# Kernel optimization log

Hardware: AMD Instinct MI355X
Metric: run time of the kernel (lower is better)

## Reference

```python
import jax, jax.numpy as jnp
import numpy as np

EPS = 1e-9          # nr.projection eps
EXPANSION = 0.5     # expansion_parts
Z_THRESH = 5.0      # interaction_threshold
B, NS, NO, P, KS, KO = 256, 10475, 65536, 8, 1024, 2048


def _make_cam_Ks(rng):
    # replicate __init__: focal = focal / bboxes[:,2:] * [192,256]; K /= 256
    wh = rng.uniform(100.0, 300.0, size=(B, 2)).astype(np.float32)
    f = 5000.0 / wh * np.array([192.0, 256.0], dtype=np.float32)
    K = np.tile(np.eye(3, dtype=np.float32), (B, 1, 1))
    K[:, 0, 0] = f[:, 0]
    K[:, 1, 1] = f[:, 1]
    K[:, 0, 2] = K[:, 1, 2] = 128.0
    return jnp.asarray(K / 256.0)


def setup_inputs() -> dict:
    key = jax.random.key(0)
    k1, k2, k3, k4 = jax.random.split(key, 4)
    rng = np.random.default_rng(0)
    return {
        "smpl_v": jax.random.normal(k1, (B, NS, 3), dtype=jnp.float32),
        "object_v": jax.random.normal(k2, (B, NO, 3), dtype=jnp.float32),
        "cam_Ks": _make_cam_Ks(rng),
        "smpl_part_idx": jax.random.randint(k3, (P, KS), 0, NS, dtype=jnp.int32),
        "object_part_idx": jax.random.randint(k4, (P, KO), 0, NO, dtype=jnp.int32),
    }


def _project(vertices, cam_Ks):
    # nr.projection with R=I, t=0, dist_coeffs=0, orig_size=1; verts pre-flipped in y
    v = vertices * jnp.array([1.0, -1.0, 1.0], dtype=vertices.dtype)
    x, y, z = v[..., 0], v[..., 1], v[..., 2]
    x_ = x / (z + EPS)
    y_ = y / (z + EPS)
    fx = cam_Ks[:, 0, 0][:, None]
    fy = cam_Ks[:, 1, 1][:, None]
    cx = cam_Ks[:, 0, 2][:, None]
    cy = cam_Ks[:, 1, 2][:, None]
    u = fx * x_ + cx
    w = 1.0 - (fy * y_ + cy)      # v = orig_size - v, orig_size = 1
    u = 2.0 * (u - 0.5)
    w = 2.0 * (w - 0.5)
    return jnp.stack([u, w], axis=-1)  # [B, N, 2]


def _part_bboxes(proj, part_idx):
    # proj [B,N,2], part_idx [P,K] -> expanded bboxes [B,P,4] (x0,y0,x1,y1)
    pv = proj[:, part_idx]                        # [B,P,K,2]
    lo = pv.min(axis=2)
    hi = pv.max(axis=2)
    center = (lo + hi) * 0.5
    half = (hi - lo) * 0.5 * (1.0 + EXPANSION)
    return jnp.concatenate([center - half, center + half], axis=-1)


def reference(smpl_v, object_v, cam_Ks, smpl_part_idx, object_part_idx):
    bsz = smpl_v.shape[0]
    # loss_inter = MSE of per-mesh centroids, divided by batch size
    loss_inter = jnp.mean((smpl_v.mean(1) - object_v.mean(1)) ** 2) / bsz

    # bbox assignment runs under torch.no_grad -> stop_gradient
    proj_s = _project(jax.lax.stop_gradient(smpl_v), cam_Ks)
    proj_o = _project(jax.lax.stop_gradient(object_v), cam_Ks)
    bb_p = _part_bboxes(proj_s, smpl_part_idx)    # [B,P,4]
    bb_o = _part_bboxes(proj_o, object_part_idx)  # [B,P,4]

    # NOTE: original indexes person_part_bboxes[object_part_name], so the 2D
    # overlap depends only on the (shared-name) object part index o -> [B,P]
    overlap = ~((bb_o[..., 0] > bb_p[..., 2]) | (bb_p[..., 0] > bb_o[..., 2])
                | (bb_o[..., 1] > bb_p[..., 3]) | (bb_p[..., 1] > bb_o[..., 3]))

    # z-range distance for every (smpl part s, object part o) pair
    sz = smpl_v[:, smpl_part_idx, 2]              # [B,Ps,Ks]
    oz = object_v[:, object_part_idx, 2]          # [B,Po,Ko]
    a = sz.min(-1)[:, :, None]                    # [B,Ps,1]
    b = sz.max(-1)[:, :, None]
    c = oz.min(-1)[:, None, :]                    # [B,1,Po]
    d = oz.max(-1)[:, None, :]
    gap = jnp.minimum(jnp.abs(c - b), jnp.abs(a - d))
    z_dist = jnp.where((d >= a) & (b >= c), 0.0, gap)       # [B,Ps,Po]

    mask = overlap[:, None, :] & (z_dist < Z_THRESH)         # [B,Ps,Po]

    smpl_means = smpl_v[:, smpl_part_idx].mean(2)            # [B,Ps,3]
    obj_means = object_v[:, object_part_idx].mean(2)         # [B,Po,3]
    pair_mse = jnp.mean(
        (smpl_means[:, :, None, :] - obj_means[:, None, :, :]) ** 2, axis=-1)
    count = mask.sum()
    loss_parts = jnp.where(count > 0,
                           (pair_mse * mask).sum() / count.astype(pair_mse.dtype),
                           jnp.zeros((), pair_mse.dtype))
    return jnp.stack([loss_inter, loss_parts])  # ('inter', 'inter_part')
```

## Files before the change

### kernel.cpp

```cpp
#include <hip/hip_runtime.h>
#include <math.h>

constexpr int B_   = 256;
constexpr int NS_  = 10475;
constexpr int NO_  = 65536;
constexpr int P_   = 8;
constexpr int KS_  = 1024;
constexpr int KO_  = 2048;
constexpr int NBLK_S = 4;
constexpr int NBLK_O = 16;
constexpr float EPS_ = 1e-9f;
constexpr float ZTH_ = 5.0f;

constexpr int UNITS_PER_B = NBLK_O + P_ + NBLK_S + P_;
constexpr int NXCD = 8;
constexpr int B_PER_XCD = B_ / NXCD;

#define DEV_INLINE __device__ __forceinline__

DEV_INLINE float wredsum(float v) {
#pragma unroll
    for (int o = 32; o; o >>= 1) v += __shfl_down(v, o);
    return v;
}
DEV_INLINE float wredmin(float v) {
#pragma unroll
    for (int o = 32; o; o >>= 1) v = fminf(v, __shfl_down(v, o));
    return v;
}
DEV_INLINE float wredmax(float v) {
#pragma unroll
    for (int o = 32; o; o >>= 1) v = fmaxf(v, __shfl_down(v, o));
    return v;
}

template <int N, int NBLK>
DEV_INLINE void batch_sum_body(const float* __restrict__ v, int b, int blk,
                               float* __restrict__ out) {
    const int chunk = (N + NBLK - 1) / NBLK;
    const int s = blk * chunk;
    const int e = min(N, s + chunk);
    const float* base = v + (size_t)b * N * 3;
    float sx = 0.f, sy = 0.f, sz = 0.f;
    for (int i = s + (int)threadIdx.x; i < e; i += 256) {
        const float* p = base + (size_t)i * 3;
        sx += p[0];
        sy += p[1];
        sz += p[2];
    }
    __shared__ float red[3][4];
    float r0 = wredsum(sx), r1 = wredsum(sy), r2 = wredsum(sz);
    const int lane = threadIdx.x & 63, wv = threadIdx.x >> 6;
    if (lane == 0) { red[0][wv] = r0; red[1][wv] = r1; red[2][wv] = r2; }
    __syncthreads();
    if (threadIdx.x == 0) {
        float* o = out + ((size_t)b * NBLK + blk) * 3;
        o[0] = red[0][0] + red[0][1] + red[0][2] + red[0][3];
        o[1] = red[1][0] + red[1][1] + red[1][2] + red[1][3];
        o[2] = red[2][0] + red[2][1] + red[2][2] + red[2][3];
    }
}

template <int N, int K>
DEV_INLINE void part_stats_body(const float* __restrict__ v,
                                const int* __restrict__ pidx,
                                const float* __restrict__ Ks, int b, int p,
                                float* __restrict__ out) {
    const float fx = Ks[b * 9 + 0];
    const float cx = Ks[b * 9 + 2];
    const float fy = Ks[b * 9 + 4];
    const float cy = Ks[b * 9 + 5];
    const float* base = v + (size_t)b * N * 3;
    const int* idx = pidx + (size_t)p * K;

    float umin = INFINITY, umax = -INFINITY, wmin = INFINITY, wmax = -INFINITY;
    float zmin = INFINITY, zmax = -INFINITY;
    float sx = 0.f, sy = 0.f, sz = 0.f;

    constexpr int ITER = K / 256;
    int ids[ITER];
#pragma unroll
    for (int j = 0; j < ITER; ++j) ids[j] = idx[threadIdx.x + j * 256];

#pragma unroll
    for (int j = 0; j < ITER; ++j) {
        const float* vp = base + (size_t)ids[j] * 3;
        const float x = vp[0], y = vp[1], z = vp[2];
        sx += x; sy += y; sz += z;
        zmin = fminf(zmin, z); zmax = fmaxf(zmax, z);
        float u, w;
        {
#pragma clang fp contract(off)
            const float zd = z + EPS_;
            const float x_ = x / zd;
            const float y_ = (-y) / zd;
            u = fx * x_ + cx;
            w = 1.0f - (fy * y_ + cy);
            u = 2.0f * (u - 0.5f);
            w = 2.0f * (w - 0.5f);
        }
        umin = fminf(umin, u); umax = fmaxf(umax, u);
        wmin = fminf(wmin, w); wmax = fmaxf(wmax, w);
    }

    __shared__ float red[4][9];
    float r[9];
    r[0] = wredmin(umin); r[1] = wredmax(umax);
    r[2] = wredmin(wmin); r[3] = wredmax(wmax);
    r[4] = wredmin(zmin); r[5] = wredmax(zmax);
    r[6] = wredsum(sx);   r[7] = wredsum(sy); r[8] = wredsum(sz);
    const int lane = threadIdx.x & 63, wv = threadIdx.x >> 6;
    if (lane == 0) {
#pragma unroll
        for (int q = 0; q < 9; ++q) red[wv][q] = r[q];
    }
    __syncthreads();
    if (threadIdx.x == 0) {
        float* o = out + ((size_t)b * P_ + p) * 9;
        o[0] = fminf(fminf(red[0][0], red[1][0]), fminf(red[2][0], red[3][0]));
        o[1] = fmaxf(fmaxf(red[0][1], red[1][1]), fmaxf(red[2][1], red[3][1]));
        o[2] = fminf(fminf(red[0][2], red[1][2]), fminf(red[2][2], red[3][2]));
        o[3] = fmaxf(fmaxf(red[0][3], red[1][3]), fmaxf(red[2][3], red[3][3]));
        o[4] = fminf(fminf(red[0][4], red[1][4]), fminf(red[2][4], red[3][4]));
        o[5] = fmaxf(fmaxf(red[0][5], red[1][5]), fmaxf(red[2][5], red[3][5]));
        o[6] = red[0][6] + red[1][6] + red[2][6] + red[3][6];
        o[7] = red[0][7] + red[1][7] + red[2][7] + red[3][7];
        o[8] = red[0][8] + red[1][8] + red[2][8] + red[3][8];
    }
}

__global__ __launch_bounds__(256) void phase1_kernel(
        const float* __restrict__ obj, const float* __restrict__ smpl,
        const float* __restrict__ Ks,
        const int* __restrict__ sidx, const int* __restrict__ oidx,
        float* __restrict__ sumO, float* __restrict__ sumS,
        float* __restrict__ statsO, float* __restrict__ statsS) {
    const int gid = blockIdx.x;
    const int xcd = gid & (NXCD - 1);
    const int unit = gid >> 3;
    const int b = (unit / UNITS_PER_B) * NXCD + xcd;
    const int role = unit % UNITS_PER_B;
    if (role < NBLK_O) {
        batch_sum_body<NO_, NBLK_O>(obj, b, role, sumO);
    } else if (role < NBLK_O + P_) {
        part_stats_body<NO_, KO_>(obj, oidx, Ks, b, role - NBLK_O, statsO);
    } else if (role < NBLK_O + P_ + NBLK_S) {
        batch_sum_body<NS_, NBLK_S>(smpl, b, role - (NBLK_O + P_), sumS);
    } else {
        part_stats_body<NS_, KS_>(smpl, sidx, Ks, b, role - (NBLK_O + P_ + NBLK_S), statsS);
    }
}

__global__ __launch_bounds__(64) void pair_kernel(
        const float* __restrict__ statsS, const float* __restrict__ statsO,
        float* __restrict__ partial) {
#pragma clang fp contract(off)
    const int b = blockIdx.x;
    __shared__ float sS[P_][9];
    __shared__ float sO[P_][9];
    const int t = threadIdx.x;
    for (int i = t; i < 2 * P_ * 9; i += 64) {
        if (i < P_ * 9) sS[i / 9][i % 9] = statsS[(size_t)b * P_ * 9 + i];
        else {
            const int u = i - P_ * 9;
            sO[u / 9][u % 9] = statsO[(size_t)b * P_ * 9 + u];
        }
    }
    __syncthreads();

    const int ps = t >> 3;
    const int po = t & 7;

    const float* ssp = sS[po];
    const float* sop = sO[po];
    const float pcu = (ssp[0] + ssp[1]) * 0.5f;
    const float phu = (ssp[1] - ssp[0]) * 0.5f * 1.5f;
    const float pcw = (ssp[2] + ssp[3]) * 0.5f;
    const float phw = (ssp[3] - ssp[2]) * 0.5f * 1.5f;
    const float px0 = pcu - phu, px1 = pcu + phu;
    const float py0 = pcw - phw, py1 = pcw + phw;
    const float ocu = (sop[0] + sop[1]) * 0.5f;
    const float ohu = (sop[1] - sop[0]) * 0.5f * 1.5f;
    const float ocw = (sop[2] + sop[3]) * 0.5f;
    const float ohw = (sop[3] - sop[2]) * 0.5f * 1.5f;
    const float ox0 = ocu - ohu, ox1 = ocu + ohu;
    const float oy0 = ocw - ohw, oy1 = ocw + ohw;
    const bool ov = !((ox0 > px1) || (px0 > ox1) || (oy0 > py1) || (py0 > oy1));

    const float a  = sS[ps][4];
    const float bm = sS[ps][5];
    const float c  = sO[po][4];
    const float d  = sO[po][5];
    const float gap = fminf(fabsf(c - bm), fabsf(a - d));
    const float zd = ((d >= a) && (bm >= c)) ? 0.f : gap;
    const bool m = ov && (zd < ZTH_);

    const float ms0 = sS[ps][6] / (float)KS_;
    const float ms1 = sS[ps][7] / (float)KS_;
    const float ms2 = sS[ps][8] / (float)KS_;
    const float mo0 = sO[po][6] / (float)KO_;
    const float mo1 = sO[po][7] / (float)KO_;
    const float mo2 = sO[po][8] / (float)KO_;
    const float d0 = ms0 - mo0, d1 = ms1 - mo1, d2 = ms2 - mo2;
    const float pm = (d0 * d0 + d1 * d1 + d2 * d2) / 3.0f;

    float psum = m ? pm : 0.f;
    float pcnt = m ? 1.f : 0.f;
    psum = wredsum(psum);
    pcnt = wredsum(pcnt);
    if (t == 0) {
        partial[(size_t)b * 2 + 0] = psum;
        partial[(size_t)b * 2 + 1] = pcnt;
    }
}

__global__ __launch_bounds__(256) void last_kernel(
        const float* __restrict__ sumS, const float* __restrict__ sumO,
        const float* __restrict__ pairPartial, float* __restrict__ out) {
    const int t = threadIdx.x;
    float d2 = 0.f;
#pragma unroll
    for (int c = 0; c < 3; ++c) {
        float ss = 0.f, so = 0.f;
#pragma unroll
        for (int k = 0; k < NBLK_S; ++k) ss += sumS[((size_t)t * NBLK_S + k) * 3 + c];
#pragma unroll
        for (int k = 0; k < NBLK_O; ++k) so += sumO[((size_t)t * NBLK_O + k) * 3 + c];
        const float ms = ss / (float)NS_;
        const float mo = so / (float)NO_;
        const float d = ms - mo;
        d2 += d * d;
    }
    float s = pairPartial[(size_t)t * 2 + 0];
    float c2 = pairPartial[(size_t)t * 2 + 1];
    __shared__ float rli[4], rs[4], rc[4];
    const float rl = wredsum(d2);
    const float ss2 = wredsum(s);
    const float cc = wredsum(c2);
    const int lane = t & 63, wv = t >> 6;
    if (lane == 0) { rli[wv] = rl; rs[wv] = ss2; rc[wv] = cc; }
    __syncthreads();
    if (t == 0) {
        const float tot = rli[0] + rli[1] + rli[2] + rli[3];
        out[0] = tot / (3.0f * (float)B_) / (float)B_;
        const float S = rs[0] + rs[1] + rs[2] + rs[3];
        const float C = rc[0] + rc[1] + rc[2] + rc[3];
        out[1] = (C > 0.f) ? (S / C) : 0.f;
    }
}

extern "C" void kernel_launch(void* const* d_in, const int* in_sizes, int n_in,
                              void* d_out, int out_size, void* d_ws, size_t ws_size,
                              hipStream_t stream) {
    const float* smpl = (const float*)d_in[0];
    const float* obj  = (const float*)d_in[1];
    const float* Ks   = (const float*)d_in[2];
    const int*   sidx = (const int*)d_in[3];
    const int*   oidx = (const int*)d_in[4];
    float* out = (float*)d_out;

    float* w = (float*)d_ws;
    float* sumO   = w;
    float* sumS   = sumO + (size_t)B_ * NBLK_O * 3;
    float* statsS = sumS + (size_t)B_ * NBLK_S * 3;
    float* statsO = statsS + (size_t)B_ * P_ * 9;
    float* pairP  = statsO + (size_t)B_ * P_ * 9;

    phase1_kernel<<<B_ * UNITS_PER_B, 256, 0, stream>>>(
        obj, smpl, Ks, sidx, oidx, sumO, sumS, statsO, statsS);
    pair_kernel<<<B_, 64, 0, stream>>>(statsS, statsO, pairP);
    last_kernel<<<1, 256, 0, stream>>>(sumS, sumO, pairP, out);
}
```

Baseline: 69.85 us.

## Bucket part indices per vertex chunk and gather part stats from LDS-staged chunks

```diff
diff --git a/kernel.cpp b/kernel.cpp
--- a/kernel.cpp
+++ b/kernel.cpp
@@ -7,14 +7,17 @@
 constexpr int P_   = 8;
 constexpr int KS_  = 1024;
 constexpr int KO_  = 2048;
-constexpr int NBLK_S = 4;
-constexpr int NBLK_O = 16;
 constexpr float EPS_ = 1e-9f;
 constexpr float ZTH_ = 5.0f;
 
-constexpr int UNITS_PER_B = NBLK_O + P_ + NBLK_S + P_;
-constexpr int NXCD = 8;
-constexpr int B_PER_XCD = B_ / NXCD;
+constexpr int CO_   = 2048;
+constexpr int NCO_  = NO_ / CO_;
+constexpr int CS_   = 1310;
+constexpr int NCS_  = 8;
+constexpr int CAPO_ = 256;
+constexpr int CAPS_ = 512;
+constexpr int VPTO_ = CO_ / 256;
+constexpr int VPTS_ = (CS_ + 255) / 256;
 
 #define DEV_INLINE __device__ __forceinline__
 
@@ -34,136 +37,186 @@
     return v;
 }
 
-template <int N, int NBLK>
-DEV_INLINE void batch_sum_body(const float* __restrict__ v, int b, int blk,
-                               float* __restrict__ out) {
-    const int chunk = (N + NBLK - 1) / NBLK;
-    const int s = blk * chunk;
-    const int e = min(N, s + chunk);
-    const float* base = v + (size_t)b * N * 3;
+__global__ __launch_bounds__(256) void bucket_build_kernel(
+        const int* __restrict__ sidx, const int* __restrict__ oidx,
+        int* __restrict__ objCnt, int* __restrict__ objBkt,
+        int* __restrict__ smplCnt, int* __restrict__ smplBkt) {
+    const int t = threadIdx.x;
+    __shared__ int scan[256];
+    __shared__ int sbase, stot;
+    int K; const int* list; int c0, c1; int* bkt; int* cntp;
+    if (blockIdx.x < NCO_ * P_) {
+        const int c = blockIdx.x % NCO_;
+        const int p = blockIdx.x / NCO_;
+        K = KO_; list = oidx + (size_t)p * KO_;
+        c0 = c * CO_; c1 = c0 + CO_;
+        bkt = objBkt + (size_t)(c * P_ + p) * CAPO_;
+        cntp = objCnt + (c * P_ + p);
+    } else {
+        const int u = blockIdx.x - NCO_ * P_;
+        const int c = u % NCS_;
+        const int p = u / NCS_;
+        K = KS_; list = sidx + (size_t)p * KS_;
+        c0 = c * CS_; c1 = min(c0 + CS_, NS_);
+        bkt = smplBkt + (size_t)(c * P_ + p) * CAPS_;
+        cntp = smplCnt + (c * P_ + p);
+    }
+    if (t == 0) sbase = 0;
+    __syncthreads();
+    for (int seg = 0; seg < K; seg += 256) {
+        const int k = seg + t;
+        const int v = (k < K) ? list[k] : -1;
+        const int flag = (v >= c0 && v < c1) ? 1 : 0;
+        scan[t] = flag;
+        __syncthreads();
+#pragma unroll
+        for (int off = 1; off < 256; off <<= 1) {
+            const int x = (t >= off) ? scan[t - off] : 0;
+            __syncthreads();
+            scan[t] += x;
+            __syncthreads();
+        }
+        if (flag) bkt[sbase + scan[t] - 1] = v - c0;
+        if (t == 255) stot = scan[255];
+        __syncthreads();
+        if (t == 0) sbase += stot;
+        __syncthreads();
+    }
+    if (t == 0) *cntp = sbase;
+}
+
+template <int N, int CHUNK, int NCH, int CAP, int VPT>
+DEV_INLINE void chunk_body(const float* __restrict__ v,
+                           const float* __restrict__ Ks,
+                           const int* __restrict__ cnt,
+                           const int* __restrict__ bkt,
+                           const int b, const int c,
+                           float* __restrict__ sums,
+                           float* __restrict__ part,
+                           float* lds, float (*red)[4]) {
+    const int t = threadIdx.x;
+    const int c0 = c * CHUNK;
+    const int cn = min(CHUNK, N - c0);
+    const float* base = v + ((size_t)b * N + (size_t)c0) * 3;
     float sx = 0.f, sy = 0.f, sz = 0.f;
-    for (int i = s + (int)threadIdx.x; i < e; i += 256) {
-        const float* p = base + (size_t)i * 3;
-        sx += p[0];
-        sy += p[1];
-        sz += p[2];
-    }
-    __shared__ float red[3][4];
-    float r0 = wredsum(sx), r1 = wredsum(sy), r2 = wredsum(sz);
-    const int lane = threadIdx.x & 63, wv = threadIdx.x >> 6;
+#pragma unroll
+    for (int j = 0; j < VPT; ++j) {
+        const int i = j * 256 + t;
+        if (i < cn) {
+            const float* p = base + (size_t)i * 3;
+            const float x = p[0], y = p[1], z = p[2];
+            sx += x; sy += y; sz += z;
+            lds[i * 3 + 0] = x; lds[i * 3 + 1] = y; lds[i * 3 + 2] = z;
+        }
+    }
+    const int lane = t & 63, wv = t >> 6;
+    const float r0 = wredsum(sx), r1 = wredsum(sy), r2 = wredsum(sz);
     if (lane == 0) { red[0][wv] = r0; red[1][wv] = r1; red[2][wv] = r2; }
     __syncthreads();
-    if (threadIdx.x == 0) {
-        float* o = out + ((size_t)b * NBLK + blk) * 3;
+    if (t == 0) {
+        float* o = sums + ((size_t)b * NCH + c) * 3;
         o[0] = red[0][0] + red[0][1] + red[0][2] + red[0][3];
         o[1] = red[1][0] + red[1][1] + red[1][2] + red[1][3];
         o[2] = red[2][0] + red[2][1] + red[2][2] + red[2][3];
     }
-}
-
-template <int N, int K>
-DEV_INLINE void part_stats_body(const float* __restrict__ v,
-                                const int* __restrict__ pidx,
-                                const float* __restrict__ Ks, int b, int p,
-                                float* __restrict__ out) {
     const float fx = Ks[b * 9 + 0];
     const float cx = Ks[b * 9 + 2];
     const float fy = Ks[b * 9 + 4];
     const float cy = Ks[b * 9 + 5];
-    const float* base = v + (size_t)b * N * 3;
-    const int* idx = pidx + (size_t)p * K;
-
-    float umin = INFINITY, umax = -INFINITY, wmin = INFINITY, wmax = -INFINITY;
-    float zmin = INFINITY, zmax = -INFINITY;
-    float sx = 0.f, sy = 0.f, sz = 0.f;
-
-    constexpr int ITER = K / 256;
-    int ids[ITER];
-#pragma unroll
-    for (int j = 0; j < ITER; ++j) ids[j] = idx[threadIdx.x + j * 256];
-
-#pragma unroll
-    for (int j = 0; j < ITER; ++j) {
-        const float* vp = base + (size_t)ids[j] * 3;
-        const float x = vp[0], y = vp[1], z = vp[2];
-        sx += x; sy += y; sz += z;
-        zmin = fminf(zmin, z); zmax = fmaxf(zmax, z);
-        float u, w;
-        {
+#pragma unroll
+    for (int pi = 0; pi < 2; ++pi) {
+        const int pp = wv + pi * 4;
+        const int bc = cnt[c * P_ + pp];
+        const int* bl = bkt + (size_t)(c * P_ + pp) * CAP;
+        float umin = INFINITY, umax = -INFINITY;
+        float wmin = INFINITY, wmax = -INFINITY;
+        float zmn = INFINITY, zmx = -INFINITY;
+        float psx = 0.f, psy = 0.f, psz = 0.f;
+        for (int e = lane; e < bc; e += 64) {
+            const int li = bl[e];
+            const float x = lds[li * 3 + 0];
+            const float y = lds[li * 3 + 1];
+            const float z = lds[li * 3 + 2];
+            psx += x; psy += y; psz += z;
+            zmn = fminf(zmn, z); zmx = fmaxf(zmx, z);
+            float u, w;
+            {
 #pragma clang fp contract(off)
-            const float zd = z + EPS_;
-            const float x_ = x / zd;
-            const float y_ = (-y) / zd;
-            u = fx * x_ + cx;
-            w = 1.0f - (fy * y_ + cy);
-            u = 2.0f * (u - 0.5f);
-            w = 2.0f * (w - 0.5f);
-        }
-        umin = fminf(umin, u); umax = fmaxf(umax, u);
-        wmin = fminf(wmin, w); wmax = fmaxf(wmax, w);
-    }
-
-    __shared__ float red[4][9];
-    float r[9];
-    r[0] = wredmin(umin); r[1] = wredmax(umax);
-    r[2] = wredmin(wmin); r[3] = wredmax(wmax);
-    r[4] = wredmin(zmin); r[5] = wredmax(zmax);
-    r[6] = wredsum(sx);   r[7] = wredsum(sy); r[8] = wredsum(sz);
-    const int lane = threadIdx.x & 63, wv = threadIdx.x >> 6;
-    if (lane == 0) {
-#pragma unroll
-        for (int q = 0; q < 9; ++q) red[wv][q] = r[q];
-    }
-    __syncthreads();
-    if (threadIdx.x == 0) {
-        float* o = out + ((size_t)b * P_ + p) * 9;
-        o[0] = fminf(fminf(red[0][0], red[1][0]), fminf(red[2][0], red[3][0]));
-        o[1] = fmaxf(fmaxf(red[0][1], red[1][1]), fmaxf(red[2][1], red[3][1]));
-        o[2] = fminf(fminf(red[0][2], red[1][2]), fminf(red[2][2], red[3][2]));
-        o[3] = fmaxf(fmaxf(red[0][3], red[1][3]), fmaxf(red[2][3], red[3][3]));
-        o[4] = fminf(fminf(red[0][4], red[1][4]), fminf(red[2][4], red[3][4]));
-        o[5] = fmaxf(fmaxf(red[0][5], red[1][5]), fmaxf(red[2][5], red[3][5]));
-        o[6] = red[0][6] + red[1][6] + red[2][6] + red[3][6];
-        o[7] = red[0][7] + red[1][7] + red[2][7] + red[3][7];
-        o[8] = red[0][8] + red[1][8] + red[2][8] + red[3][8];
+                const float zd = z + EPS_;
+                const float x_ = x / zd;
+                const float y_ = (-y) / zd;
+                u = fx * x_ + cx;
+                w = 1.0f - (fy * y_ + cy);
+                u = 2.0f * (u - 0.5f);
+                w = 2.0f * (w - 0.5f);
+            }
+            umin = fminf(umin, u); umax = fmaxf(umax, u);
+            wmin = fminf(wmin, w); wmax = fmaxf(wmax, w);
+        }
+        float r[9];
+        r[0] = wredmin(umin); r[1] = wredmax(umax);
+        r[2] = wredmin(wmin); r[3] = wredmax(wmax);
+        r[4] = wredmin(zmn);  r[5] = wredmax(zmx);
+        r[6] = wredsum(psx);  r[7] = wredsum(psy); r[8] = wredsum(psz);
+        if (lane == 0) {
+            float* o = part + (((size_t)b * NCH + c) * P_ + pp) * 9;
+#pragma unroll
+            for (int q = 0; q < 9; ++q) o[q] = r[q];
+        }
     }
 }
 
 __global__ __launch_bounds__(256) void phase1_kernel(
         const float* __restrict__ obj, const float* __restrict__ smpl,
         const float* __restrict__ Ks,
-        const int* __restrict__ sidx, const int* __restrict__ oidx,
+        const int* __restrict__ objCnt, const int* __restrict__ objBkt,
+        const int* __restrict__ smplCnt, const int* __restrict__ smplBkt,
         float* __restrict__ sumO, float* __restrict__ sumS,
-        float* __restrict__ statsO, float* __restrict__ statsS) {
+        float* __restrict__ partO, float* __restrict__ partS) {
+    __shared__ float lds[CO_ * 3];
+    __shared__ float red[3][4];
     const int gid = blockIdx.x;
-    const int xcd = gid & (NXCD - 1);
-    const int unit = gid >> 3;
-    const int b = (unit / UNITS_PER_B) * NXCD + xcd;
-    const int role = unit % UNITS_PER_B;
-    if (role < NBLK_O) {
-        batch_sum_body<NO_, NBLK_O>(obj, b, role, sumO);
-    } else if (role < NBLK_O + P_) {
-        part_stats_body<NO_, KO_>(obj, oidx, Ks, b, role - NBLK_O, statsO);
-    } else if (role < NBLK_O + P_ + NBLK_S) {
-        batch_sum_body<NS_, NBLK_S>(smpl, b, role - (NBLK_O + P_), sumS);
+    if (gid < B_ * NCO_) {
+        const int b = gid / NCO_, c = gid % NCO_;
+        chunk_body<NO_, CO_, NCO_, CAPO_, VPTO_>(obj, Ks, objCnt, objBkt, b, c,
+                                                 sumO, partO, lds, red);
     } else {
-        part_stats_body<NS_, KS_>(smpl, sidx, Ks, b, role - (NBLK_O + P_ + NBLK_S), statsS);
-    }
-}
-
-__global__ __launch_bounds__(64) void pair_kernel(
-        const float* __restrict__ statsS, const float* __restrict__ statsO,
-        float* __restrict__ partial) {
+        const int u = gid - B_ * NCO_;
+        const int b = u / NCS_, c = u % NCS_;
+        chunk_body<NS_, CS_, NCS_, CAPS_, VPTS_>(smpl, Ks, smplCnt, smplBkt, b, c,
+                                                 sumS, partS, lds, red);
+    }
+}
+
+__global__ __launch_bounds__(64) void finish_kernel(
+        const float* __restrict__ partS, const float* __restrict__ partO,
+        float* __restrict__ pairPartial) {
 #pragma clang fp contract(off)
     const int b = blockIdx.x;
+    const int t = threadIdx.x;
     __shared__ float sS[P_][9];
     __shared__ float sO[P_][9];
-    const int t = threadIdx.x;
-    for (int i = t; i < 2 * P_ * 9; i += 64) {
-        if (i < P_ * 9) sS[i / 9][i % 9] = statsS[(size_t)b * P_ * 9 + i];
-        else {
-            const int u = i - P_ * 9;
-            sO[u / 9][u % 9] = statsO[(size_t)b * P_ * 9 + u];
+    for (int q = t; q < 72; q += 64) {
+        const int s = q / 8, p = q % 8;
+        const bool isMin = (s == 0 || s == 2 || s == 4);
+        const bool isMax = (s == 1 || s == 3 || s == 5);
+        {
+            const float* po = partO + (size_t)b * NCO_ * 72 + p * 9 + s;
+            float acc = isMin ? INFINITY : (isMax ? -INFINITY : 0.f);
+            for (int k = 0; k < NCO_; ++k) {
+                const float vv = po[(size_t)k * 72];
+                acc = isMin ? fminf(acc, vv) : (isMax ? fmaxf(acc, vv) : acc + vv);
+            }
+            sO[p][s] = acc;
+        }
+        {
+            const float* ps = partS + (size_t)b * NCS_ * 72 + p * 9 + s;
+            float acc = isMin ? INFINITY : (isMax ? -INFINITY : 0.f);
+            for (int k = 0; k < NCS_; ++k) {
+                const float vv = ps[(size_t)k * 72];
+                acc = isMin ? fminf(acc, vv) : (isMax ? fmaxf(acc, vv) : acc + vv);
+            }
+            sS[p][s] = acc;
         }
     }
     __syncthreads();
@@ -209,8 +262,8 @@
     psum = wredsum(psum);
     pcnt = wredsum(pcnt);
     if (t == 0) {
-        partial[(size_t)b * 2 + 0] = psum;
-        partial[(size_t)b * 2 + 1] = pcnt;
+        pairPartial[(size_t)b * 2 + 0] = psum;
+        pairPartial[(size_t)b * 2 + 1] = pcnt;
     }
 }
 
@@ -223,9 +276,9 @@
     for (int c = 0; c < 3; ++c) {
         float ss = 0.f, so = 0.f;
 #pragma unroll
-        for (int k = 0; k < NBLK_S; ++k) ss += sumS[((size_t)t * NBLK_S + k) * 3 + c];
-#pragma unroll
-        for (int k = 0; k < NBLK_O; ++k) so += sumO[((size_t)t * NBLK_O + k) * 3 + c];
+        for (int k = 0; k < NCS_; ++k) ss += sumS[((size_t)t * NCS_ + k) * 3 + c];
+#pragma unroll
+        for (int k = 0; k < NCO_; ++k) so += sumO[((size_t)t * NCO_ + k) * 3 + c];
         const float ms = ss / (float)NS_;
         const float mo = so / (float)NO_;
         const float d = ms - mo;
@@ -259,15 +312,21 @@
     const int*   oidx = (const int*)d_in[4];
     float* out = (float*)d_out;
 
-    float* w = (float*)d_ws;
-    float* sumO   = w;
-    float* sumS   = sumO + (size_t)B_ * NBLK_O * 3;
-    float* statsS = sumS + (size_t)B_ * NBLK_S * 3;
-    float* statsO = statsS + (size_t)B_ * P_ * 9;
-    float* pairP  = statsO + (size_t)B_ * P_ * 9;
-
-    phase1_kernel<<<B_ * UNITS_PER_B, 256, 0, stream>>>(
-        obj, smpl, Ks, sidx, oidx, sumO, sumS, statsO, statsS);
-    pair_kernel<<<B_, 64, 0, stream>>>(statsS, statsO, pairP);
+    int* objCnt  = (int*)d_ws;
+    int* smplCnt = objCnt + 256;
+    int* objBkt  = objCnt + 512;
+    int* smplBkt = objBkt + NCO_ * P_ * CAPO_;
+    float* sumO  = (float*)(smplBkt + NCS_ * P_ * CAPS_);
+    float* sumS  = sumO + (size_t)B_ * NCO_ * 3;
+    float* partO = sumS + (size_t)B_ * NCS_ * 3;
+    float* partS = partO + (size_t)B_ * NCO_ * 72;
+    float* pairP = partS + (size_t)B_ * NCS_ * 72;
+
+    bucket_build_kernel<<<NCO_ * P_ + NCS_ * P_, 256, 0, stream>>>(
+        sidx, oidx, objCnt, objBkt, smplCnt, smplBkt);
+    phase1_kernel<<<B_ * NCO_ + B_ * NCS_, 256, 0, stream>>>(
+        obj, smpl, Ks, objCnt, objBkt, smplCnt, smplBkt,
+        sumO, sumS, partO, partS);
+    finish_kernel<<<B_, 64, 0, stream>>>(partS, partO, pairP);
     last_kernel<<<1, 256, 0, stream>>>(sumS, sumO, pairP, out);
 }
```

Result: slower. 112.1 us (+60.5%).
